# Performance work log

Measured on AMD Instinct MI355X. Metric: run time of the kernel, lower is better.

## Reference

```python
import jax, jax.numpy as jnp
import numpy as np

B, NC, F, U = 8, 64, 8, 128   # batch, mesh size, ConvLSTM filters, LSTM units
NITER = 4
BS = 200.0                    # box size
B1, B2, LR, EPS = 0.9, 0.999, 0.1, 1e-7


def _conv3d(x, w, b=None):
    out = jax.lax.conv_general_dilated(x, w, (1, 1, 1), 'SAME',
                                       dimension_numbers=('NDHWC', 'DHWIO', 'NDHWC'))
    return out if b is None else out + b


def _conv1d(x, w, b):
    return jax.lax.conv_general_dilated(x, w, (1,), 'SAME',
                                        dimension_numbers=('NWC', 'WIO', 'NWC')) + b


def setup_inputs():
    key = jax.random.key(0)
    ks = jax.random.split(key, 16)
    # radial |k| bin map, values in [0, NC)
    kf = np.fft.fftfreq(NC) * NC
    kx, ky, kz = np.meshgrid(kf, kf, kf, indexing='ij')
    knorm = np.sqrt(kx ** 2 + ky ** 2 + kz ** 2)
    kbinmap = np.minimum((knorm / knorm.max() * (NC - 1)).astype(np.int32), NC - 1)
    s = 0.05
    return {
        'x_init': jax.random.normal(ks[0], (B, NC, NC, NC), jnp.float32),
        'y':      jax.random.normal(ks[1], (B, NC, NC, NC), jnp.float32),
        'x_true': jax.random.normal(ks[2], (B, NC, NC, NC), jnp.float32),
        'kbinmap': jnp.asarray(kbinmap),
        # input_layer: Conv3D 2 -> F
        'W_in': jax.random.normal(ks[3], (3, 3, 3, 2, F), jnp.float32) * s,
        'b_in': jnp.zeros((F,), jnp.float32),
        # ConvLSTM3D cell: gates order i,f,g,o
        'Wx3': jax.random.normal(ks[4], (3, 3, 3, F, 4 * F), jnp.float32) * s,
        'Wh3': jax.random.normal(ks[5], (3, 3, 3, F, 4 * F), jnp.float32) * s,
        'b3':  jnp.zeros((4 * F,), jnp.float32),
        # output_layer: Conv3D F -> 1
        'W_out': jax.random.normal(ks[6], (3, 3, 3, F, 1), jnp.float32) * s,
        'b_out': jnp.zeros((1,), jnp.float32),
        # input_layer1d: Dense 2*NC -> U
        'Wd1': jax.random.normal(ks[7], (2 * NC, U), jnp.float32) * s,
        'bd1': jnp.zeros((U,), jnp.float32),
        # LSTM cell (units U)
        'Wlx': jax.random.normal(ks[8], (U, 4 * U), jnp.float32) * s,
        'Wlh': jax.random.normal(ks[9], (U, 4 * U), jnp.float32) * s,
        'bl':  jnp.zeros((4 * U,), jnp.float32),
        # output_layer1d: Dense U -> NC
        'Wd2': jax.random.normal(ks[10], (U, NC), jnp.float32) * s,
        'bd2': jnp.zeros((NC,), jnp.float32),
        # output_layer1dconv: Conv1D 1 -> 1, kernel 3
        'Wc1': jax.random.normal(ks[11], (3, 1, 1), jnp.float32) * s,
        'bc1': jnp.zeros((1,), jnp.float32),
    }


def _forward(x_init, y, x_true, W_in, b_in, Wx3, Wh3, b3, W_out, b_out,
             Wd1, bd1, Wlx, Wlh, bl, Wd2, bd2, Wc1, bc1, kbinmap):
    nc = x_init.shape[-1]
    bsz = x_init.shape[0]
    kflat = kbinmap.reshape(-1)
    counts = jax.ops.segment_sum(jnp.ones(kflat.shape, jnp.float32), kflat,
                                 num_segments=nc)

    def varmap(x):
        # tfvarmap: binned power spectrum, [B, nc]
        pm = jnp.abs(jnp.fft.fftn(x, axes=(1, 2, 3)) / nc ** 3) ** 2
        pmf = pm.reshape(bsz, -1)
        power = jax.vmap(lambda p: jax.ops.segment_sum(p, kflat, num_segments=nc))(pmf)
        return power / counts

    def filt(x, ps, p):
        # colorps (p=+0.5) / whitenps (p=-0.5); flowpm r2c/c2r norms cancel
        pmesh = ps[:, kbinmap]                      # [B,nc,nc,nc] gather by kbin
        fac = (pmesh ** p).astype(jnp.complex64)
        return jnp.real(jnp.fft.ifftn(jnp.fft.fftn(x, axes=(1, 2, 3)) * fac,
                                      axes=(1, 2, 3)))

    def convlstm(x, h, c):
        z = _conv3d(x, Wx3, b3) + _conv3d(h, Wh3)
        i, f, g, o = jnp.split(z, 4, axis=-1)
        c = jax.nn.sigmoid(f) * c + jax.nn.sigmoid(i) * jnp.tanh(g)
        h = jax.nn.sigmoid(o) * jnp.tanh(c)
        return h, c

    def lstm(x, h, c):
        z = x @ Wlx + h @ Wlh + bl
        i, f, g, o = jnp.split(z, 4, axis=-1)
        c = jax.nn.sigmoid(f) * c + jax.nn.sigmoid(i) * jnp.tanh(g)
        h = jax.nn.sigmoid(o) * jnp.tanh(c)
        return h, c

    ln10 = jnp.log(jnp.float32(10.0))

    def step(carry, t):
        pos, m, v, h1, c1, h3, c3, loss = carry
        grad = pos - y                              # stand-in grad_fn (data-consistency)
        m = B1 * m + (1.0 - B1) * grad
        v = B2 * v + (1.0 - B2) * grad * grad
        mc = m / (1.0 - B1 ** t)
        vc = v / (1.0 - B2 ** t)
        delta = -LR * mc / (jnp.sqrt(vc) + EPS)
        pspos = varmap(pos)
        psdelta = varmap(delta)
        lpspos = jnp.log(pspos * BS ** 3) / ln10
        lpsdelta = jnp.log(psdelta * BS ** 3) / ln10
        # 3D branch
        cell_in = _conv3d(jnp.stack([pos, delta], axis=-1), W_in, b_in)
        h3, c3 = convlstm(cell_in, h3, c3)
        delta_poswhite = _conv3d(h3, W_out, b_out)[..., 0]
        # 1D power-spectrum branch
        x1 = jnp.concatenate([lpspos, lpsdelta], axis=-1) @ Wd1 + bd1
        h1, c1 = lstm(x1, h1, c1)
        lps = h1 @ Wd2 + bd2
        lps = _conv1d(lps[..., None], Wc1, bc1)[..., 0]
        psdeltanew = jnp.exp(lps)                   # note: exp (base e), as in source
        new_pos = pos + filt(delta_poswhite, psdeltanew, 0.5)
        loss = loss + jnp.mean((x_true - new_pos) ** 2)
        return (new_pos, m, v, h1, c1, h3, c3, loss), None

    z = jnp.zeros_like(x_init)
    init = (x_init, z, z,
            jnp.zeros((bsz, U), x_init.dtype), jnp.zeros((bsz, U), x_init.dtype),
            jnp.zeros(x_init.shape + (F,), x_init.dtype),
            jnp.zeros(x_init.shape + (F,), x_init.dtype),
            jnp.zeros((), x_init.dtype))
    ts = jnp.arange(1, NITER + 1, dtype=jnp.float32)
    (pos, m, v, h1, c1, h3, c3, loss), _ = jax.lax.scan(step, init, ts)
    return pos, loss


def reference(x_init, y, x_true, kbinmap, W_in, b_in, Wx3, Wh3, b3, W_out, b_out,
              Wd1, bd1, Wlx, Wlh, bl, Wd2, bd2, Wc1, bc1):
    return _forward(x_init, y, x_true, W_in, b_in, Wx3, Wh3, b3, W_out, b_out,
                    Wd1, bd1, Wlx, Wlh, bl, Wd2, bd2, Wc1, bc1, kbinmap)
```

## Files before the change

### kernel.cpp

```cpp
#include <hip/hip_runtime.h>
#include <math.h>

#define NCC 64
#define NB 8
#define VOL (NCC*NCC*NCC)
#define TOT (NB*VOL)
#define WTOT 170869
#define PI2 6.2831853071795864769f
#define HS 287496
#define SX 4356

typedef unsigned short u16;
typedef __bf16 bf16x8 __attribute__((ext_vector_type(8)));
typedef float f32x16 __attribute__((ext_vector_type(16)));

__device__ __forceinline__ float b2f(u16 h){ return __uint_as_float(((unsigned)h)<<16); }
__device__ __forceinline__ u16 f2b(float f){
  unsigned u = __float_as_uint(f);
  unsigned r = (u + 0x7FFFu + ((u>>16)&1u)) >> 16;
  return (u16)r;
}
__device__ __forceinline__ float fsig(float x){ return 1.f / (1.f + __expf(-x)); }
__device__ __forceinline__ float ftanh(float x){
  float e = __expf(2.f * x);
  return 1.f - 2.f / (e + 1.f);
}

template<bool INV>
__device__ __forceinline__ void fft8(float2* x) {
  const float C = 0.70710678118654752440f;
  float2 s0,s1,s2,s3,s4,s5,s6,s7;
  s0 = make_float2(x[0].x + x[4].x, x[0].y + x[4].y);
  s4 = make_float2(x[0].x - x[4].x, x[0].y - x[4].y);
  s1 = make_float2(x[1].x + x[5].x, x[1].y + x[5].y);
  s5 = make_float2(x[1].x - x[5].x, x[1].y - x[5].y);
  s2 = make_float2(x[2].x + x[6].x, x[2].y + x[6].y);
  s6 = make_float2(x[2].x - x[6].x, x[2].y - x[6].y);
  s3 = make_float2(x[3].x + x[7].x, x[3].y + x[7].y);
  s7 = make_float2(x[3].x - x[7].x, x[3].y - x[7].y);
  float2 n5, n6, n7;
  if (!INV) {
    n5 = make_float2(C*(s5.x + s5.y), C*(s5.y - s5.x));
    n6 = make_float2(s6.y, -s6.x);
    n7 = make_float2(C*(s7.y - s7.x), -C*(s7.x + s7.y));
  } else {
    n5 = make_float2(C*(s5.x - s5.y), C*(s5.y + s5.x));
    n6 = make_float2(-s6.y, s6.x);
    n7 = make_float2(-C*(s7.x + s7.y), C*(s7.x - s7.y));
  }
  float2 t0,t1,t2,t3,t4,t5,t6,t7,d;
  t0 = make_float2(s0.x + s2.x, s0.y + s2.y);
  t2 = make_float2(s0.x - s2.x, s0.y - s2.y);
  t1 = make_float2(s1.x + s3.x, s1.y + s3.y);
  d  = make_float2(s1.x - s3.x, s1.y - s3.y);
  t3 = INV ? make_float2(-d.y, d.x) : make_float2(d.y, -d.x);
  t4 = make_float2(s4.x + n6.x, s4.y + n6.y);
  t6 = make_float2(s4.x - n6.x, s4.y - n6.y);
  t5 = make_float2(n5.x + n7.x, n5.y + n7.y);
  d  = make_float2(n5.x - n7.x, n5.y - n7.y);
  t7 = INV ? make_float2(-d.y, d.x) : make_float2(d.y, -d.x);
  x[0] = make_float2(t0.x + t1.x, t0.y + t1.y);
  x[1] = make_float2(t0.x - t1.x, t0.y - t1.y);
  x[2] = make_float2(t2.x + t3.x, t2.y + t3.y);
  x[3] = make_float2(t2.x - t3.x, t2.y - t3.y);
  x[4] = make_float2(t4.x + t5.x, t4.y + t5.y);
  x[5] = make_float2(t4.x - t5.x, t4.y - t5.y);
  x[6] = make_float2(t6.x + t7.x, t6.y + t7.y);
  x[7] = make_float2(t6.x - t7.x, t6.y - t7.y);
}

template<bool INV>
__device__ __forceinline__ void dft64(float2* Pf, const float2* tw, int ls, int ns) {
  const int BR[8] = {0,4,2,6,1,5,3,7};
  int t = threadIdx.x;
  int L0 = t >> 3, b = t & 7, L1 = L0 + 32;
  float2 v0[8], v1[8];
  #pragma unroll
  for (int a = 0; a < 8; ++a) v0[a] = Pf[L0*ls + (8*a + b)*ns];
  #pragma unroll
  for (int a = 0; a < 8; ++a) v1[a] = Pf[L1*ls + (8*a + b)*ns];
  __syncthreads();
  fft8<INV>(v0); fft8<INV>(v1);
  #pragma unroll
  for (int r = 0; r < 8; ++r) {
    float2 w = tw[(b * r) & 63];
    if (INV) w.y = -w.y;
    float2 a0 = v0[BR[r]], a1 = v1[BR[r]];
    Pf[L0*ls + (8*b + r)*ns] = make_float2(a0.x*w.x - a0.y*w.y, a0.x*w.y + a0.y*w.x);
    Pf[L1*ls + (8*b + r)*ns] = make_float2(a1.x*w.x - a1.y*w.y, a1.x*w.y + a1.y*w.x);
  }
  __syncthreads();
  int r = t & 7;
  #pragma unroll
  for (int q = 0; q < 8; ++q) v0[q] = Pf[L0*ls + (8*q + r)*ns];
  #pragma unroll
  for (int q = 0; q < 8; ++q) v1[q] = Pf[L1*ls + (8*q + r)*ns];
  fft8<INV>(v0); fft8<INV>(v1);
  #pragma unroll
  for (int j = 0; j < 8; ++j) {
    Pf[L0*ls + (8*BR[j] + r)*ns] = v0[j];
    Pf[L1*ls + (8*BR[j] + r)*ns] = v1[j];
  }
  __syncthreads();
}

__global__ __launch_bounds__(256) void k_sniff(const u16* __restrict__ x, int* __restrict__ flag) {
  __shared__ int cnt;
  if (threadIdx.x == 0) cnt = 0;
  __syncthreads();
  int sane = 0;
  for (int i = threadIdx.x; i < 1024; i += 256) {
    u16 h = x[2 * i];
    int e = (h >> 7) & 0xFF;
    if (h == 0 || (e >= 0x68 && e <= 0x8F)) sane++;
  }
  atomicAdd(&cnt, sane);
  __syncthreads();
  if (threadIdx.x == 0) flag[0] = (cnt >= 768) ? 1 : 0;
}

__global__ __launch_bounds__(256) void k_cvt(const void* __restrict__ in, size_t eoff,
                                             float* __restrict__ out, const int* __restrict__ flag) {
  size_t i = (size_t)blockIdx.x * 256 + threadIdx.x;
  if (*flag) out[i] = b2f(((const u16*)in)[eoff + i]);
  else       out[i] = ((const float*)in)[eoff + i];
}

__global__ __launch_bounds__(256) void k_cvtall(
    const void* s0, const void* s1, const void* s2, const void* s3,
    const void* s4, const void* s5, const void* s6, const void* s7,
    const void* s8, const void* s9, const void* s10, const void* s11,
    const void* s12, const void* s13, const void* s14, const void* s15,
    float* __restrict__ out, const int* __restrict__ flag) {
  const void* ps[16] = {s0,s1,s2,s3,s4,s5,s6,s7,s8,s9,s10,s11,s12,s13,s14,s15};
  const int offs[17] = {0,432,440,7352,14264,14296,14512,14513,30897,31025,
                        96561,162097,162609,170801,170865,170868,170869};
  int i = blockIdx.x * 256 + threadIdx.x;
  if (i >= WTOT) return;
  int s = 0;
  #pragma unroll
  for (int k = 1; k < 16; ++k) if (i >= offs[k]) s = k;
  int j = i - offs[s];
  if (*flag) out[i] = b2f(((const u16*)ps[s])[j]);
  else       out[i] = ((const float*)ps[s])[j];
}

__global__ __launch_bounds__(256) void k_mkwf(const void* __restrict__ Wx, const void* __restrict__ Wh,
                                              const int* __restrict__ flag, u16* __restrict__ Wf) {
  int i = blockIdx.x * 256 + threadIdx.x;
  if (i >= 13824) return;
  int j = i & 7, co = (i >> 3) & 31, hi = (i >> 8) & 1, tap = i >> 9;
  int src = tap * 256 + j * 32 + co;
  const void* P = hi ? Wh : Wx;
  u16 val;
  if (*flag) val = ((const u16*)P)[src];
  else       val = f2b(((const float*)P)[src]);
  Wf[i] = val;
}

__global__ __launch_bounds__(256) void k_counts(const int* __restrict__ kbin,
                                                float* __restrict__ cnts) {
  __shared__ float s[NCC];
  int t = threadIdx.x;
  if (t < NCC) s[t] = 0.f;
  __syncthreads();
  int i = blockIdx.x * 256 + t;
  atomicAdd(&s[kbin[i]], 1.f);
  __syncthreads();
  if (t < NCC) atomicAdd(&cnts[t], s[t]);
}

__global__ __launch_bounds__(256) void k_fft_zy_adam(
    const float* __restrict__ pos, const void* __restrict__ yraw, size_t yoff,
    float* __restrict__ m, float* __restrict__ v, float* __restrict__ dpw,
    float2* __restrict__ cout, float ib1, float ib2, int first,
    const int* __restrict__ flag) {
  __shared__ float2 P[64*66];
  __shared__ float2 tw[64];
  int t = threadIdx.x;
  if (t < 64) { float s, c; __sincosf(-(PI2/64.f)*(float)t, &s, &c); tw[t] = make_float2(c, s); }
  size_t pb = (size_t)blockIdx.x * 4096;
  int bf = *flag;
  #pragma unroll
  for (int i = 0; i < 4; ++i) {
    int i4 = t + 256*i;
    float4 p4 = ((const float4*)(pos + pb))[i4];
    float yv[4];
    if (bf) {
      uint2 yu = ((const uint2*)((const u16*)yraw + yoff + pb))[i4];
      const u16* yp = (const u16*)&yu;
      yv[0]=b2f(yp[0]); yv[1]=b2f(yp[1]); yv[2]=b2f(yp[2]); yv[3]=b2f(yp[3]);
    } else {
      float4 y4 = ((const float4*)((const float*)yraw + yoff + pb))[i4];
      yv[0]=y4.x; yv[1]=y4.y; yv[2]=y4.z; yv[3]=y4.w;
    }
    float pv[4] = {p4.x, p4.y, p4.z, p4.w};
    float mo[4], vo[4], dd[4];
    if (!first) {
      float4 m4 = ((const float4*)(m + pb))[i4];
      float4 v4 = ((const float4*)(v + pb))[i4];
      mo[0]=m4.x; mo[1]=m4.y; mo[2]=m4.z; mo[3]=m4.w;
      vo[0]=v4.x; vo[1]=v4.y; vo[2]=v4.z; vo[3]=v4.w;
    }
    #pragma unroll
    for (int c = 0; c < 4; ++c) {
      float g = pv[c] - yv[c];
      float mi = first ? 0.1f*g : 0.9f*mo[c] + 0.1f*g;
      float vi = first ? 0.001f*g*g : 0.999f*vo[c] + 0.001f*g*g;
      mo[c] = mi; vo[c] = vi;
      dd[c] = -0.1f * (mi * ib1) / (sqrtf(vi * ib2) + 1e-7f);
    }
    ((float4*)(m + pb))[i4]   = make_float4(mo[0], mo[1], mo[2], mo[3]);
    ((float4*)(v + pb))[i4]   = make_float4(vo[0], vo[1], vo[2], vo[3]);
    ((float4*)(dpw + pb))[i4] = make_float4(dd[0], dd[1], dd[2], dd[3]);
    int base = i4 * 4;
    float2* row = P + (base >> 6)*66 + (base & 63);
    row[0] = make_float2(pv[0], 0.f);
    row[1] = make_float2(pv[1], 0.f);
    row[2] = make_float2(pv[2], 0.f);
    row[3] = make_float2(pv[3], 0.f);
  }
  __syncthreads();
  dft64<false>(P, tw, 66, 1);
  dft64<false>(P, tw, 1, 66);
  float4* dst = (float4*)(cout + pb);
  #pragma unroll
  for (int i = 0; i < 8; ++i) {
    int idx2 = (t + 256*i) * 2;
    float2 a = P[(idx2 >> 6)*66 + (idx2 & 63)];
    float2 b = P[(idx2 >> 6)*66 + (idx2 & 63) + 1];
    dst[t + 256*i] = make_float4(a.x, a.y, b.x, b.y);
  }
}

__global__ __launch_bounds__(256) void k_fft_zy(const float* __restrict__ rin,
                                                float2* __restrict__ cout) {
  __shared__ float2 P[64*66];
  __shared__ float2 tw[64];
  int t = threadIdx.x;
  if (t < 64) { float s, c; __sincosf(-(PI2/64.f)*(float)t, &s, &c); tw[t] = make_float2(c, s); }
  const float* src = rin + (size_t)blockIdx.x * 4096;
  #pragma unroll
  for (int i = 0; i < 4; ++i) {
    float4 v = ((const float4*)src)[t + 256*i];
    int base = (t + 256*i) * 4;
    float2* row = P + (base >> 6)*66 + (base & 63);
    row[0] = make_float2(v.x, 0.f);
    row[1] = make_float2(v.y, 0.f);
    row[2] = make_float2(v.z, 0.f);
    row[3] = make_float2(v.w, 0.f);
  }
  __syncthreads();
  dft64<false>(P, tw, 66, 1);
  dft64<false>(P, tw, 1, 66);
  float4* dst = (float4*)(cout + (size_t)blockIdx.x * 4096);
  #pragma unroll
  for (int i = 0; i < 8; ++i) {
    int idx2 = (t + 256*i) * 2;
    float2 a = P[(idx2 >> 6)*66 + (idx2 & 63)];
    float2 b = P[(idx2 >> 6)*66 + (idx2 & 63) + 1];
    dst[t + 256*i] = make_float4(a.x, a.y, b.x, b.y);
  }
}

__global__ __launch_bounds__(256) void k_fft_x_pow(const float2* __restrict__ cin,
                                                   const int* __restrict__ kb,
                                                   float* __restrict__ psum) {
  __shared__ float2 P[64*66];
  __shared__ float2 tw[64];
  __shared__ float pb[64];
  int t = threadIdx.x;
  if (t < 64) { float s, c; __sincosf(-(PI2/64.f)*(float)t, &s, &c); tw[t] = make_float2(c, s); pb[t] = 0.f; }
  int b = blockIdx.x >> 6, y = blockIdx.x & 63;
  #pragma unroll
  for (int i = 0; i < 8; ++i) {
    int idx2 = (t + 256*i) * 2;
    int x = idx2 >> 6, z = idx2 & 63;
    float4 v = *(const float4*)(cin + (((size_t)(b*64 + x)*64 + y)*64 + z));
    P[x*66 + z]     = make_float2(v.x, v.y);
    P[x*66 + z + 1] = make_float2(v.z, v.w);
  }
  __syncthreads();
  dft64<false>(P, tw, 1, 66);
  const float INV2 = 1.0f / ((float)VOL * (float)VOL);
  #pragma unroll
  for (int i = 0; i < 16; ++i) {
    int idx = t + 256*i;
    int x = idx >> 6, z = idx & 63;
    float2 a = P[x*66 + z];
    float pm = (a.x*a.x + a.y*a.y) * INV2;
    atomicAdd(&pb[kb[(x*64 + y)*64 + z]], pm);
  }
  __syncthreads();
  if (t < 64) atomicAdd(&psum[b*64 + t], pb[t]);
}

__global__ __launch_bounds__(256) void k_fft_x_filt(float2* __restrict__ cb,
                                                    const int* __restrict__ kb,
                                                    const float* __restrict__ psn) {
  __shared__ float2 P[64*66];
  __shared__ float2 tw[64];
  int t = threadIdx.x;
  if (t < 64) { float s, c; __sincosf(-(PI2/64.f)*(float)t, &s, &c); tw[t] = make_float2(c, s); }
  int b = blockIdx.x >> 6, y = blockIdx.x & 63;
  #pragma unroll
  for (int i = 0; i < 8; ++i) {
    int idx2 = (t + 256*i) * 2;
    int x = idx2 >> 6, z = idx2 & 63;
    float4 v = *(const float4*)(cb + (((size_t)(b*64 + x)*64 + y)*64 + z));
    P[x*66 + z]     = make_float2(v.x, v.y);
    P[x*66 + z + 1] = make_float2(v.z, v.w);
  }
  __syncthreads();
  dft64<false>(P, tw, 1, 66);
  #pragma unroll
  for (int i = 0; i < 16; ++i) {
    int idx = t + 256*i;
    int x = idx >> 6, z = idx & 63;
    float fac = sqrtf(psn[b*64 + kb[(x*64 + y)*64 + z]]);
    float2 a = P[x*66 + z];
    P[x*66 + z] = make_float2(a.x * fac, a.y * fac);
  }
  __syncthreads();
  dft64<true>(P, tw, 1, 66);
  #pragma unroll
  for (int i = 0; i < 8; ++i) {
    int idx2 = (t + 256*i) * 2;
    int x = idx2 >> 6, z = idx2 & 63;
    float2 a = P[x*66 + z], c = P[x*66 + z + 1];
    *(float4*)(cb + (((size_t)(b*64 + x)*64 + y)*64 + z)) = make_float4(a.x, a.y, c.x, c.y);
  }
}

__global__ __launch_bounds__(256) void k_fft_zy_inv(const float2* __restrict__ cin,
                                                    float* __restrict__ pos,
                                                    const void* __restrict__ xtraw, size_t xoff,
                                                    float* __restrict__ lsum,
                                                    const int* __restrict__ flag) {
  __shared__ float2 P[64*66];
  __shared__ float2 tw[64];
  __shared__ float red[256];
  int t = threadIdx.x;
  if (t < 64) { float s, c; __sincosf(-(PI2/64.f)*(float)t, &s, &c); tw[t] = make_float2(c, s); }
  size_t pb = (size_t)blockIdx.x * 4096;
  const float4* src = (const float4*)(cin + pb);
  #pragma unroll
  for (int i = 0; i < 8; ++i) {
    float4 v = src[t + 256*i];
    int idx2 = (t + 256*i) * 2;
    P[(idx2 >> 6)*66 + (idx2 & 63)]     = make_float2(v.x, v.y);
    P[(idx2 >> 6)*66 + (idx2 & 63) + 1] = make_float2(v.z, v.w);
  }
  __syncthreads();
  dft64<true>(P, tw, 1, 66);
  dft64<true>(P, tw, 66, 1);
  float* pdst = pos + pb;
  int bf = *flag;
  float lacc = 0.f;
  #pragma unroll
  for (int i = 0; i < 16; ++i) {
    int idx = t + 256*i;
    float np = pdst[idx] + P[(idx >> 6)*66 + (idx & 63)].x * (1.0f/(float)VOL);
    pdst[idx] = np;
    float xt = bf ? b2f(((const u16*)xtraw)[xoff + pb + idx])
                  : ((const float*)xtraw)[xoff + pb + idx];
    float d = xt - np;
    lacc = fmaf(d, d, lacc);
  }
  red[t] = lacc; __syncthreads();
  for (int s = 128; s > 0; s >>= 1) { if (t < s) red[t] += red[t+s]; __syncthreads(); }
  if (t == 0) atomicAdd(lsum, red[0]);
}

__global__ __launch_bounds__(256) void k_cellin(const float* __restrict__ pos,
                                                const float* __restrict__ delta,
                                                const float* __restrict__ Win,
                                                const float* __restrict__ binf,
                                                u16* __restrict__ ci) {
  int id = blockIdx.x * 256 + threadIdx.x;
  int z = id & 63, yy = (id >> 6) & 63, x = (id >> 12) & 63, b = id >> 18;
  float acc[8];
  #pragma unroll
  for (int c = 0; c < 8; ++c) acc[c] = binf[c];
  #pragma unroll 1
  for (int tap = 0; tap < 27; ++tap) {
    int kd = tap / 9, kh = (tap / 3) % 3, kw = tap % 3;
    int nx = x + kd - 1, ny = yy + kh - 1, nz = z + kw - 1;
    if ((unsigned)nx >= 64u || (unsigned)ny >= 64u || (unsigned)nz >= 64u) continue;
    size_t n = (((size_t)b * 64 + nx) * 64 + ny) * 64 + nz;
    float p = pos[n], d = delta[n];
    const float* w = Win + tap * 16;
    #pragma unroll
    for (int c = 0; c < 8; ++c) acc[c] = fmaf(p, w[c], fmaf(d, w[8 + c], acc[c]));
  }
  u16 hh[8];
  #pragma unroll
  for (int c = 0; c < 8; ++c) hh[c] = f2b(acc[c]);
  size_t slot = (size_t)b * HS + (size_t)(x + 1) * SX + (yy + 1) * 66 + z + 1;
  *(uint4*)(ci + slot * 8) = *(uint4*)hh;
}

__global__ __launch_bounds__(512, 8) void k_clstm(const u16* __restrict__ ci,
                                                  const u16* __restrict__ hC,
                                                  u16* __restrict__ hN,
                                                  u16* __restrict__ c3u,
                                                  const u16* __restrict__ Wf,
                                                  const float* __restrict__ b3f) {
  __shared__ u16 wfl[13824];
  int t = threadIdx.x;
  for (int i = t; i < 1728; i += 512) ((uint4*)wfl)[i] = ((const uint4*)Wf)[i];
  int wv = t >> 6, l = t & 63, ln = l & 31, hi = l >> 5;
  int bid = blockIdx.x;
  int x = bid & 63, yq = (bid >> 6) & 15, b = bid >> 10;
  int y = yq * 4 + (wv >> 1), z0 = (wv & 1) * 32;
  size_t cslot = (size_t)b * HS + (size_t)(x + 1) * SX + (y + 1) * 66 + z0 + ln + 1;
  const u16* abase = (hi ? hC : ci) + cslot * 8;
  const u16* axm = abase - SX * 8;
  const u16* axp = abase + SX * 8;
  const u16* wbase = wfl + hi * 256 + ln * 8;
  __syncthreads();
  f32x16 acc;
  #pragma unroll
  for (int r = 0; r < 16; ++r) acc[r] = 0.f;
  #pragma unroll
  for (int tap = 0; tap < 27; ++tap) {
    const int dx = tap / 9, dy = (tap / 3) % 3 - 1, dz = tap % 3 - 1;
    const u16* ab = (dx == 0) ? axm : ((dx == 1) ? abase : axp);
    bf16x8 wfr = __builtin_bit_cast(bf16x8, *(const uint4*)(wbase + tap * 512));
    bf16x8 afr = __builtin_bit_cast(bf16x8, *(const uint4*)(ab + (dy * 66 + dz) * 8));
    acc = __builtin_amdgcn_mfma_f32_32x32x16_bf16(wfr, afr, acc, 0, 0, 0);
  }
  float4 bi  = *(const float4*)(b3f + 4 * hi);
  float4 bff = *(const float4*)(b3f + 8 + 4 * hi);
  float4 bg  = *(const float4*)(b3f + 16 + 4 * hi);
  float4 bo_ = *(const float4*)(b3f + 24 + 4 * hi);
  const float* bip = (const float*)&bi;
  const float* bfp = (const float*)&bff;
  const float* bgp = (const float*)&bg;
  const float* bop = (const float*)&bo_;
  uint2 cu = *(const uint2*)(c3u + cslot * 8 + hi * 4);
  const u16* cp = (const u16*)&cu;
  u16 cw[4], hw[4];
  #pragma unroll
  for (int q = 0; q < 4; ++q) {
    float zi  = acc[q]      + bip[q];
    float zf  = acc[4 + q]  + bfp[q];
    float zg  = acc[8 + q]  + bgp[q];
    float zo_ = acc[12 + q] + bop[q];
    float cn = fsig(zf) * b2f(cp[q]) + fsig(zi) * ftanh(zg);
    cw[q] = f2b(cn);
    hw[q] = f2b(fsig(zo_) * ftanh(cn));
  }
  *(uint2*)(c3u + cslot * 8 + hi * 4) = *(uint2*)cw;
  *(uint2*)(hN + cslot * 8 + hi * 4)  = *(uint2*)hw;
}

__global__ __launch_bounds__(256) void k_wout(const u16* __restrict__ h,
                                              const float* __restrict__ Wo,
                                              const float* __restrict__ bo,
                                              float* __restrict__ dpw) {
  int id = blockIdx.x * 256 + threadIdx.x;
  int z = id & 63, yy = (id >> 6) & 63, x = (id >> 12) & 63, b = id >> 18;
  size_t cslot = (size_t)b * HS + (size_t)(x + 1) * SX + (yy + 1) * 66 + z + 1;
  const u16* hb = h + cslot * 8;
  const u16* hxm = hb - SX * 8;
  const u16* hxp = hb + SX * 8;
  float acc = bo[0];
  #pragma unroll 1
  for (int tap = 0; tap < 27; ++tap) {
    int kd = tap / 9, kh = (tap / 3) % 3, kw = tap % 3;
    const u16* ab = (kd == 0) ? hxm : ((kd == 1) ? hb : hxp);
    uint4 a = *(const uint4*)(ab + ((kh - 1) * 66 + (kw - 1)) * 8);
    const u16* hp = (const u16*)&a;
    const float* w = Wo + tap * 8;
    #pragma unroll
    for (int c = 0; c < 8; ++c) acc = fmaf(b2f(hp[c]), w[c], acc);
  }
  dpw[id] = acc;
}

__global__ __launch_bounds__(256) void k_small(const float* __restrict__ psp,
                                               const float* __restrict__ psd,
                                               const float* __restrict__ cnts,
                                               const float* __restrict__ Wd1,
                                               const float* __restrict__ bd1,
                                               const float* __restrict__ Wlx,
                                               const float* __restrict__ Wlh,
                                               const float* __restrict__ bl,
                                               const float* __restrict__ Wd2,
                                               const float* __restrict__ bd2,
                                               const float* __restrict__ Wc1,
                                               const float* __restrict__ bc1,
                                               float* __restrict__ h1, float* __restrict__ c1,
                                               float* __restrict__ psn) {
  __shared__ float lp[128], x1[128], hs[128], zz[512], lps[66];
  int t = threadIdx.x, b = blockIdx.x;
  if (t < 64) {
    lp[t]      = __log10f(fmaxf(psp[b*64 + t] / cnts[t] * 8.0e6f, 1e-30f));
    lp[64 + t] = __log10f(fmaxf(psd[b*64 + t] / cnts[t] * 8.0e6f, 1e-30f));
  }
  if (t < 128) hs[t] = h1[b*128 + t];
  __syncthreads();
  if (t < 128) {
    float a = bd1[t];
    for (int j = 0; j < 128; ++j) a = fmaf(lp[j], Wd1[j*128 + t], a);
    x1[t] = a;
  }
  __syncthreads();
  for (int k = t; k < 512; k += 256) {
    float a = bl[k];
    for (int u = 0; u < 128; ++u)
      a = fmaf(x1[u], Wlx[u*512 + k], fmaf(hs[u], Wlh[u*512 + k], a));
    zz[k] = a;
  }
  __syncthreads();
  if (t < 128) {
    float cv = fsig(zz[128 + t]) * c1[b*128 + t] + fsig(zz[t]) * ftanh(zz[256 + t]);
    c1[b*128 + t] = cv;
    float hv = fsig(zz[384 + t]) * ftanh(cv);
    h1[b*128 + t] = hv; hs[t] = hv;
  }
  __syncthreads();
  if (t < 64) {
    float a = bd2[t];
    for (int u = 0; u < 128; ++u) a = fmaf(hs[u], Wd2[u*64 + t], a);
    lps[t + 1] = a;
  }
  __syncthreads();
  if (t < 64) {
    float a = fmaf(Wc1[1], lps[t + 1], bc1[0]);
    if (t > 0)  a = fmaf(Wc1[0], lps[t], a);
    if (t < 63) a = fmaf(Wc1[2], lps[t + 2], a);
    psn[b*64 + t] = __expf(a);
  }
}

__global__ __launch_bounds__(256) void k_out(const float* __restrict__ pos, void* __restrict__ outp,
                                             size_t eoff, const int* __restrict__ flag) {
  size_t i = (size_t)blockIdx.x * 256 + threadIdx.x;
  if (*flag) ((u16*)outp)[eoff + i] = f2b(pos[i]);
  else       ((float*)outp)[eoff + i] = pos[i];
}

__global__ void k_loss(const float* __restrict__ lsum, void* __restrict__ outp,
                       const int* __restrict__ flag) {
  float l = lsum[0] * (1.0f / (float)TOT);
  if (*flag) ((u16*)outp)[TOT] = f2b(l);
  else       ((float*)outp)[TOT] = l;
}

__global__ void k_sent(u16* __restrict__ outp) { outp[0] = f2b(1000.0f); }

extern "C" void kernel_launch(void* const* d_in, const int* in_sizes, int n_in,
                              void* d_out, int out_size, void* d_ws, size_t ws_size,
                              hipStream_t stream) {
  const void* x_init = d_in[0];
  const void* y      = d_in[1];
  const void* x_true = d_in[2];
  const int*  kbin   = (const int*)d_in[3];

  int nbs = 0;
  for (int cand = 8; cand >= 1; cand >>= 1) {
    size_t n1c = (size_t)cand * VOL;
    size_t slc = (size_t)cand * HS;
    size_t need = 4 * n1c * 4
                + 4 * slc * 16
                + n1c * 8
                + (171008 + 6912 + (size_t)cand * (192 + 256) + 96) * 4;
    if (need <= ws_size) { nbs = cand; break; }
  }
  if (nbs == 0) { k_sent<<<1, 1, 0, stream>>>((u16*)d_out); return; }

  size_t n1 = (size_t)nbs * VOL;
  size_t sl = (size_t)nbs * HS;
  float* ws   = (float*)d_ws;
  float* pos  = ws;
  float* m    = pos + n1;
  float* v    = m + n1;
  float* dpw  = v + n1;
  u16*  c3u   = (u16*)(dpw + n1);
  u16*  ci    = c3u + sl*8;
  u16*  hA    = ci + sl*8;
  u16*  hB    = hA + sl*8;
  float2* cb  = (float2*)(hB + sl*8);
  float* wbuf = (float*)((float*)cb + n1*2);
  u16*  Wf    = (u16*)(wbuf + 171008);
  float* psp  = wbuf + 171008 + 6912;
  float* psd  = psp + (size_t)nbs*64;
  float* psn  = psd + (size_t)nbs*64;
  float* cnts = psn + (size_t)nbs*64;
  float* lsum = cnts + 64;
  float* h1   = lsum + 8;
  float* c1   = h1 + (size_t)nbs*128;
  int*   flag = (int*)(c1 + (size_t)nbs*128);

  float* Win_f = wbuf + 0;     float* bin_f = wbuf + 432;
  float* b3_f  = wbuf + 14264; float* Wo_f  = wbuf + 14296;
  float* bo_f  = wbuf + 14512; float* Wd1_f = wbuf + 14513;
  float* bd1_f = wbuf + 30897; float* Wlx_f = wbuf + 31025;
  float* Wlh_f = wbuf + 96561; float* bl_f  = wbuf + 162097;
  float* Wd2_f = wbuf + 162609; float* bd2_f = wbuf + 170801;
  float* Wc1_f = wbuf + 170865; float* bc1_f = wbuf + 170868;

  const int CB = (int)(n1 / 256);

  k_sniff<<<1, 256, 0, stream>>>((const u16*)x_init, flag);
  k_cvtall<<<(WTOT + 255) / 256, 256, 0, stream>>>(
      d_in[4], d_in[5], d_in[6], d_in[7], d_in[8], d_in[9], d_in[10], d_in[11],
      d_in[12], d_in[13], d_in[14], d_in[15], d_in[16], d_in[17], d_in[18], d_in[19],
      wbuf, flag);
  k_mkwf<<<54, 256, 0, stream>>>(d_in[6], d_in[7], flag, Wf);
  hipMemsetAsync(cnts, 0, 72 * 4, stream);
  k_counts<<<VOL / 256, 256, 0, stream>>>(kbin, cnts);

  for (int b0 = 0; b0 < NB; b0 += nbs) {
    hipMemsetAsync(c3u, 0, sl * 64, stream);
    hipMemsetAsync(h1, 0, (size_t)nbs * 256 * 4, stream);
    k_cvt<<<CB, 256, 0, stream>>>(x_init, (size_t)b0 * VOL, pos, flag);

    u16* hC = hA;
    u16* hN = hB;
    for (int t = 1; t <= 4; ++t) {
      float ib1 = (float)(1.0 / (1.0 - pow(0.9, (double)t)));
      float ib2 = (float)(1.0 / (1.0 - pow(0.999, (double)t)));

      hipMemsetAsync(psp, 0, (size_t)nbs * 128 * 4, stream);
      k_fft_zy_adam<<<nbs * 64, 256, 0, stream>>>(pos, y, (size_t)b0 * VOL, m, v, dpw,
                                                  cb, ib1, ib2, t == 1, flag);
      k_fft_x_pow<<<nbs * 64, 256, 0, stream>>>(cb, kbin, psp);
      k_fft_zy<<<nbs * 64, 256, 0, stream>>>(dpw, cb);
      k_fft_x_pow<<<nbs * 64, 256, 0, stream>>>(cb, kbin, psd);

      k_cellin<<<CB, 256, 0, stream>>>(pos, dpw, Win_f, bin_f, ci);
      k_clstm<<<nbs * 1024, 512, 0, stream>>>(ci, hC, hN, c3u, Wf, b3_f);
      k_wout<<<CB, 256, 0, stream>>>(hN, Wo_f, bo_f, dpw);

      k_small<<<nbs, 256, 0, stream>>>(psp, psd, cnts, Wd1_f, bd1_f, Wlx_f, Wlh_f, bl_f,
                                       Wd2_f, bd2_f, Wc1_f, bc1_f, h1, c1, psn);

      k_fft_zy<<<nbs * 64, 256, 0, stream>>>(dpw, cb);
      k_fft_x_filt<<<nbs * 64, 256, 0, stream>>>(cb, kbin, psn);
      k_fft_zy_inv<<<nbs * 64, 256, 0, stream>>>(cb, pos, x_true, (size_t)b0 * VOL, lsum, flag);

      u16* tmp = hC; hC = hN; hN = tmp;
    }
    k_out<<<CB, 256, 0, stream>>>(pos, d_out, (size_t)b0 * VOL, flag);
  }
  k_loss<<<1, 1, 0, stream>>>(lsum, d_out, flag);
}
```

Baseline: 1.353 ms.

## Pack pos and adam delta into one complex FFT and separate spectra by symmetry

The two real fields (position and Adam update) are packed as the real and imaginary parts of one complex 3D FFT instead of running two separate FFTs. A new kernel recovers each field's spectrum from the Hermitian symmetry X[k] and conj(X[-k]), then bins the power spectra for both. This drops one zy FFT pass and one x FFT pass per iteration. In exchange it adds a full-volume write-back of the x-FFT result and a separate binning pass that does gather reads at mirrored indices.

Result: slower. 1.515 ms (+12.0%).

```diff
diff --git a/kernel.cpp b/kernel.cpp
--- a/kernel.cpp
+++ b/kernel.cpp
@@ -215,10 +215,10 @@
     ((float4*)(dpw + pb))[i4] = make_float4(dd[0], dd[1], dd[2], dd[3]);
     int base = i4 * 4;
     float2* row = P + (base >> 6)*66 + (base & 63);
-    row[0] = make_float2(pv[0], 0.f);
-    row[1] = make_float2(pv[1], 0.f);
-    row[2] = make_float2(pv[2], 0.f);
-    row[3] = make_float2(pv[3], 0.f);
+    row[0] = make_float2(pv[0], dd[0]);
+    row[1] = make_float2(pv[1], dd[1]);
+    row[2] = make_float2(pv[2], dd[2]);
+    row[3] = make_float2(pv[3], dd[3]);
   }
   __syncthreads();
   dft64<false>(P, tw, 66, 1);
@@ -263,36 +263,57 @@
   }
 }
 
-__global__ __launch_bounds__(256) void k_fft_x_pow(const float2* __restrict__ cin,
-                                                   const int* __restrict__ kb,
-                                                   float* __restrict__ psum) {
+__global__ __launch_bounds__(256) void k_fft_x_wb(float2* __restrict__ cb) {
   __shared__ float2 P[64*66];
   __shared__ float2 tw[64];
-  __shared__ float pb[64];
-  int t = threadIdx.x;
-  if (t < 64) { float s, c; __sincosf(-(PI2/64.f)*(float)t, &s, &c); tw[t] = make_float2(c, s); pb[t] = 0.f; }
+  int t = threadIdx.x;
+  if (t < 64) { float s, c; __sincosf(-(PI2/64.f)*(float)t, &s, &c); tw[t] = make_float2(c, s); }
   int b = blockIdx.x >> 6, y = blockIdx.x & 63;
   #pragma unroll
   for (int i = 0; i < 8; ++i) {
     int idx2 = (t + 256*i) * 2;
     int x = idx2 >> 6, z = idx2 & 63;
-    float4 v = *(const float4*)(cin + (((size_t)(b*64 + x)*64 + y)*64 + z));
+    float4 v = *(const float4*)(cb + (((size_t)(b*64 + x)*64 + y)*64 + z));
     P[x*66 + z]     = make_float2(v.x, v.y);
     P[x*66 + z + 1] = make_float2(v.z, v.w);
   }
   __syncthreads();
   dft64<false>(P, tw, 1, 66);
+  #pragma unroll
+  for (int i = 0; i < 8; ++i) {
+    int idx2 = (t + 256*i) * 2;
+    int x = idx2 >> 6, z = idx2 & 63;
+    float2 a = P[x*66 + z], c = P[x*66 + z + 1];
+    *(float4*)(cb + (((size_t)(b*64 + x)*64 + y)*64 + z)) = make_float4(a.x, a.y, c.x, c.y);
+  }
+}
+
+__global__ __launch_bounds__(256) void k_powsep(const float2* __restrict__ cb,
+                                                const int* __restrict__ kb,
+                                                float* __restrict__ psp,
+                                                float* __restrict__ psd) {
+  __shared__ float pbp[64], pbd[64];
+  int t = threadIdx.x;
+  if (t < 64) { pbp[t] = 0.f; pbd[t] = 0.f; }
+  __syncthreads();
+  int b = blockIdx.y;
+  int cell = blockIdx.x * 256 + t;
+  int x = cell >> 12, yy = (cell >> 6) & 63, z = cell & 63;
+  int mc = (((64 - x) & 63) * 64 + ((64 - yy) & 63)) * 64 + ((64 - z) & 63);
+  float2 A  = cb[(size_t)b * VOL + cell];
+  float2 Bm = cb[(size_t)b * VOL + mc];
+  float Br = Bm.x, Bi = -Bm.y;
+  float Pr = 0.5f * (A.x + Br), Pi = 0.5f * (A.y + Bi);
+  float Dr = 0.5f * (A.y - Bi), Di = 0.5f * (Br - A.x);
   const float INV2 = 1.0f / ((float)VOL * (float)VOL);
-  #pragma unroll
-  for (int i = 0; i < 16; ++i) {
-    int idx = t + 256*i;
-    int x = idx >> 6, z = idx & 63;
-    float2 a = P[x*66 + z];
-    float pm = (a.x*a.x + a.y*a.y) * INV2;
-    atomicAdd(&pb[kb[(x*64 + y)*64 + z]], pm);
-  }
-  __syncthreads();
-  if (t < 64) atomicAdd(&psum[b*64 + t], pb[t]);
+  int bin = kb[cell];
+  atomicAdd(&pbp[bin], (Pr*Pr + Pi*Pi) * INV2);
+  atomicAdd(&pbd[bin], (Dr*Dr + Di*Di) * INV2);
+  __syncthreads();
+  if (t < 64) {
+    atomicAdd(&psp[b*64 + t], pbp[t]);
+    atomicAdd(&psd[b*64 + t], pbd[t]);
+  }
 }
 
 __global__ __launch_bounds__(256) void k_fft_x_filt(float2* __restrict__ cb,
@@ -627,9 +648,8 @@
       hipMemsetAsync(psp, 0, (size_t)nbs * 128 * 4, stream);
       k_fft_zy_adam<<<nbs * 64, 256, 0, stream>>>(pos, y, (size_t)b0 * VOL, m, v, dpw,
                                                   cb, ib1, ib2, t == 1, flag);
-      k_fft_x_pow<<<nbs * 64, 256, 0, stream>>>(cb, kbin, psp);
-      k_fft_zy<<<nbs * 64, 256, 0, stream>>>(dpw, cb);
-      k_fft_x_pow<<<nbs * 64, 256, 0, stream>>>(cb, kbin, psd);
+      k_fft_x_wb<<<nbs * 64, 256, 0, stream>>>(cb);
+      k_powsep<<<dim3(VOL / 256, nbs), 256, 0, stream>>>(cb, kbin, psp, psd);
 
       k_cellin<<<CB, 256, 0, stream>>>(pos, dpw, Win_f, bin_f, ci);
       k_clstm<<<nbs * 1024, 512, 0, stream>>>(ci, hC, hN, c3u, Wf, b3_f);
```

## Run output conv on MFMA, fuse power-spectrum zeroing and final output write

Applied to the files above, without the earlier changes.

The output 3D convolution (F->1) is rewritten to use bf16 MFMA 32x32x16 instructions, with a padded weight matrix pre-packed into bf16 and staged in LDS. Only one of the 32 output columns carries real weights, so most of the MFMA work is padding. The per-step memset of the power-spectrum accumulators is folded into the first FFT kernel. The separate output-copy kernel is removed, and the last inverse FFT step writes the final positions directly. Together these cut launches and scalar FMA work, at the cost of bf16 rounding of the conv weights in the fp32 path.

Result: faster. 1.294 ms (-4.4%).

```diff
diff --git a/kernel.cpp b/kernel.cpp
--- a/kernel.cpp
+++ b/kernel.cpp
@@ -158,6 +158,20 @@
   Wf[i] = val;
 }
 
+__global__ __launch_bounds__(256) void k_mkwfo(const void* __restrict__ Wo,
+                                               const int* __restrict__ flag, u16* __restrict__ Wfo) {
+  int i = blockIdx.x * 256 + threadIdx.x;
+  if (i >= 7168) return;
+  int j = i & 7, co = (i >> 3) & 31, hi = (i >> 8) & 1, p = i >> 9;
+  int tap = 2 * p + hi;
+  u16 val = 0;
+  if (co == 0 && tap < 27) {
+    int src = tap * 8 + j;
+    val = *flag ? ((const u16*)Wo)[src] : f2b(((const float*)Wo)[src]);
+  }
+  Wfo[i] = val;
+}
+
 __global__ __launch_bounds__(256) void k_counts(const int* __restrict__ kbin,
                                                 float* __restrict__ cnts) {
   __shared__ float s[NCC];
@@ -174,11 +188,16 @@
     const float* __restrict__ pos, const void* __restrict__ yraw, size_t yoff,
     float* __restrict__ m, float* __restrict__ v, float* __restrict__ dpw,
     float2* __restrict__ cout, float ib1, float ib2, int first,
-    const int* __restrict__ flag) {
+    const int* __restrict__ flag, float* __restrict__ psp, float* __restrict__ psd) {
   __shared__ float2 P[64*66];
   __shared__ float2 tw[64];
   int t = threadIdx.x;
   if (t < 64) { float s, c; __sincosf(-(PI2/64.f)*(float)t, &s, &c); tw[t] = make_float2(c, s); }
+  int bb = blockIdx.x >> 6, xx = blockIdx.x & 63;
+  if (xx == 0) {
+    if (t < 64)                 psp[bb*64 + t] = 0.f;
+    else if (t < 128)           psd[bb*64 + (t - 64)] = 0.f;
+  }
   size_t pb = (size_t)blockIdx.x * 4096;
   int bf = *flag;
   #pragma unroll
@@ -336,7 +355,8 @@
                                                     float* __restrict__ pos,
                                                     const void* __restrict__ xtraw, size_t xoff,
                                                     float* __restrict__ lsum,
-                                                    const int* __restrict__ flag) {
+                                                    const int* __restrict__ flag,
+                                                    void* __restrict__ outp, size_t ooff) {
   __shared__ float2 P[64*66];
   __shared__ float2 tw[64];
   __shared__ float red[256];
@@ -362,6 +382,10 @@
     int idx = t + 256*i;
     float np = pdst[idx] + P[(idx >> 6)*66 + (idx & 63)].x * (1.0f/(float)VOL);
     pdst[idx] = np;
+    if (outp) {
+      if (bf) ((u16*)outp)[ooff + pb + idx] = f2b(np);
+      else    ((float*)outp)[ooff + pb + idx] = np;
+    }
     float xt = bf ? b2f(((const u16*)xtraw)[xoff + pb + idx])
                   : ((const float*)xtraw)[xoff + pb + idx];
     float d = xt - np;
@@ -455,28 +479,39 @@
   *(uint2*)(hN + cslot * 8 + hi * 4)  = *(uint2*)hw;
 }
 
-__global__ __launch_bounds__(256) void k_wout(const u16* __restrict__ h,
-                                              const float* __restrict__ Wo,
-                                              const float* __restrict__ bo,
-                                              float* __restrict__ dpw) {
-  int id = blockIdx.x * 256 + threadIdx.x;
-  int z = id & 63, yy = (id >> 6) & 63, x = (id >> 12) & 63, b = id >> 18;
-  size_t cslot = (size_t)b * HS + (size_t)(x + 1) * SX + (yy + 1) * 66 + z + 1;
-  const u16* hb = h + cslot * 8;
-  const u16* hxm = hb - SX * 8;
-  const u16* hxp = hb + SX * 8;
-  float acc = bo[0];
-  #pragma unroll 1
-  for (int tap = 0; tap < 27; ++tap) {
-    int kd = tap / 9, kh = (tap / 3) % 3, kw = tap % 3;
-    const u16* ab = (kd == 0) ? hxm : ((kd == 1) ? hb : hxp);
-    uint4 a = *(const uint4*)(ab + ((kh - 1) * 66 + (kw - 1)) * 8);
-    const u16* hp = (const u16*)&a;
-    const float* w = Wo + tap * 8;
-    #pragma unroll
-    for (int c = 0; c < 8; ++c) acc = fmaf(b2f(hp[c]), w[c], acc);
-  }
-  dpw[id] = acc;
+__global__ __launch_bounds__(512, 8) void k_wout(const u16* __restrict__ h,
+                                                 const u16* __restrict__ Wfo,
+                                                 const float* __restrict__ bo,
+                                                 float* __restrict__ dpw) {
+  __shared__ u16 wfl[7168];
+  int t = threadIdx.x;
+  for (int i = t; i < 896; i += 512) ((uint4*)wfl)[i] = ((const uint4*)Wfo)[i];
+  int wv = t >> 6, l = t & 63, ln = l & 31, hi = l >> 5;
+  int bid = blockIdx.x;
+  int x = bid & 63, yq = (bid >> 6) & 15, b = bid >> 10;
+  int y = yq * 4 + (wv >> 1), z0 = (wv & 1) * 32;
+  size_t cslot = (size_t)b * HS + (size_t)(x + 1) * SX + (y + 1) * 66 + z0 + ln + 1;
+  const u16* abase = h + cslot * 8;
+  const u16* wbase = wfl + hi * 256 + ln * 8;
+  __syncthreads();
+  f32x16 acc;
+  #pragma unroll
+  for (int r = 0; r < 16; ++r) acc[r] = 0.f;
+  #pragma unroll
+  for (int p = 0; p < 14; ++p) {
+    const int t0 = 2 * p;
+    const int t1 = (2 * p + 1 < 27) ? (2 * p + 1) : 26;
+    const int o0 = (t0 / 9) * SX + ((t0 / 3) % 3) * 66 + (t0 % 3) - (SX + 66 + 1);
+    const int o1 = (t1 / 9) * SX + ((t1 / 3) % 3) * 66 + (t1 % 3) - (SX + 66 + 1);
+    int off = hi ? o1 : o0;
+    bf16x8 wfr = __builtin_bit_cast(bf16x8, *(const uint4*)(wbase + p * 512));
+    bf16x8 afr = __builtin_bit_cast(bf16x8, *(const uint4*)(abase + (ptrdiff_t)off * 8));
+    acc = __builtin_amdgcn_mfma_f32_32x32x16_bf16(wfr, afr, acc, 0, 0, 0);
+  }
+  if (hi == 0) {
+    size_t vox = (((size_t)b * 64 + x) * 64 + y) * 64 + z0 + ln;
+    dpw[vox] = acc[0] + bo[0];
+  }
 }
 
 __global__ __launch_bounds__(256) void k_small(const float* __restrict__ psp,
@@ -535,13 +570,6 @@
   }
 }
 
-__global__ __launch_bounds__(256) void k_out(const float* __restrict__ pos, void* __restrict__ outp,
-                                             size_t eoff, const int* __restrict__ flag) {
-  size_t i = (size_t)blockIdx.x * 256 + threadIdx.x;
-  if (*flag) ((u16*)outp)[eoff + i] = f2b(pos[i]);
-  else       ((float*)outp)[eoff + i] = pos[i];
-}
-
 __global__ void k_loss(const float* __restrict__ lsum, void* __restrict__ outp,
                        const int* __restrict__ flag) {
   float l = lsum[0] * (1.0f / (float)TOT);
@@ -566,7 +594,7 @@
     size_t need = 4 * n1c * 4
                 + 4 * slc * 16
                 + n1c * 8
-                + (171008 + 6912 + (size_t)cand * (192 + 256) + 96) * 4;
+                + (171008 + 6912 + 3584 + (size_t)cand * (192 + 256) + 96) * 4;
     if (need <= ws_size) { nbs = cand; break; }
   }
   if (nbs == 0) { k_sent<<<1, 1, 0, stream>>>((u16*)d_out); return; }
@@ -585,7 +613,8 @@
   float2* cb  = (float2*)(hB + sl*8);
   float* wbuf = (float*)((float*)cb + n1*2);
   u16*  Wf    = (u16*)(wbuf + 171008);
-  float* psp  = wbuf + 171008 + 6912;
+  u16*  Wfo   = Wf + 13824;
+  float* psp  = wbuf + 171008 + 6912 + 3584;
   float* psd  = psp + (size_t)nbs*64;
   float* psn  = psd + (size_t)nbs*64;
   float* cnts = psn + (size_t)nbs*64;
@@ -595,7 +624,7 @@
   int*   flag = (int*)(c1 + (size_t)nbs*128);
 
   float* Win_f = wbuf + 0;     float* bin_f = wbuf + 432;
-  float* b3_f  = wbuf + 14264; float* Wo_f  = wbuf + 14296;
+  float* b3_f  = wbuf + 14264;
   float* bo_f  = wbuf + 14512; float* Wd1_f = wbuf + 14513;
   float* bd1_f = wbuf + 30897; float* Wlx_f = wbuf + 31025;
   float* Wlh_f = wbuf + 96561; float* bl_f  = wbuf + 162097;
@@ -610,6 +639,7 @@
       d_in[12], d_in[13], d_in[14], d_in[15], d_in[16], d_in[17], d_in[18], d_in[19],
       wbuf, flag);
   k_mkwf<<<54, 256, 0, stream>>>(d_in[6], d_in[7], flag, Wf);
+  k_mkwfo<<<28, 256, 0, stream>>>(d_in[9], flag, Wfo);
   hipMemsetAsync(cnts, 0, 72 * 4, stream);
   k_counts<<<VOL / 256, 256, 0, stream>>>(kbin, cnts);
 
@@ -624,27 +654,27 @@
       float ib1 = (float)(1.0 / (1.0 - pow(0.9, (double)t)));
       float ib2 = (float)(1.0 / (1.0 - pow(0.999, (double)t)));
 
-      hipMemsetAsync(psp, 0, (size_t)nbs * 128 * 4, stream);
       k_fft_zy_adam<<<nbs * 64, 256, 0, stream>>>(pos, y, (size_t)b0 * VOL, m, v, dpw,
-                                                  cb, ib1, ib2, t == 1, flag);
+                                                  cb, ib1, ib2, t == 1, flag, psp, psd);
       k_fft_x_pow<<<nbs * 64, 256, 0, stream>>>(cb, kbin, psp);
       k_fft_zy<<<nbs * 64, 256, 0, stream>>>(dpw, cb);
       k_fft_x_pow<<<nbs * 64, 256, 0, stream>>>(cb, kbin, psd);
 
       k_cellin<<<CB, 256, 0, stream>>>(pos, dpw, Win_f, bin_f, ci);
       k_clstm<<<nbs * 1024, 512, 0, stream>>>(ci, hC, hN, c3u, Wf, b3_f);
-      k_wout<<<CB, 256, 0, stream>>>(hN, Wo_f, bo_f, dpw);
+      k_wout<<<nbs * 1024, 512, 0, stream>>>(hN, Wfo, bo_f, dpw);
 
       k_small<<<nbs, 256, 0, stream>>>(psp, psd, cnts, Wd1_f, bd1_f, Wlx_f, Wlh_f, bl_f,
                                        Wd2_f, bd2_f, Wc1_f, bc1_f, h1, c1, psn);
 
       k_fft_zy<<<nbs * 64, 256, 0, stream>>>(dpw, cb);
       k_fft_x_filt<<<nbs * 64, 256, 0, stream>>>(cb, kbin, psn);
-      k_fft_zy_inv<<<nbs * 64, 256, 0, stream>>>(cb, pos, x_true, (size_t)b0 * VOL, lsum, flag);
+      k_fft_zy_inv<<<nbs * 64, 256, 0, stream>>>(cb, pos, x_true, (size_t)b0 * VOL, lsum,
+                                                 flag, (t == 4) ? d_out : nullptr,
+                                                 (size_t)b0 * VOL);
 
       u16* tmp = hC; hC = hN; hN = tmp;
     }
-    k_out<<<CB, 256, 0, stream>>>(pos, d_out, (size_t)b0 * VOL, flag);
   }
   k_loss<<<1, 1, 0, stream>>>(lsum, d_out, flag);
 }
```
